# Performance work log

Measured on AMD Instinct MI355X. Metric: run time of the kernel, lower is better.

The kernel has to match this reference:

```python
import jax, jax.numpy as jnp
import numpy as np

D_MODEL = 1024
NUM_HEADS = 16
DEPTH = D_MODEL // NUM_HEADS
MAX_LEN = 5000


def _make_pe(d_model=D_MODEL, max_len=MAX_LEN):
    # Faithful to torch PositionalEncoding: pe shape [max_len, 1, d_model]
    position = np.arange(max_len, dtype=np.float32)[:, None]
    div_term = np.exp(np.arange(0, d_model, 2, dtype=np.float32) * (-np.log(10000.0) / d_model))
    pe = np.zeros((max_len, d_model), dtype=np.float32)
    pe[:, 0::2] = np.sin(position * div_term)
    pe[:, 1::2] = np.cos(position * div_term)
    return jnp.asarray(pe[:, None, :])  # [max_len, 1, d_model]


def setup_inputs() -> dict:
    key = jax.random.key(0)
    ks = jax.random.split(key, 11)
    B, S, D = 4, 2048, D_MODEL
    s = 1.0 / np.sqrt(D)
    inp = {
        "v": jax.random.normal(ks[0], (B, S, D), jnp.float32),
        "k": jax.random.normal(ks[1], (B, S, D), jnp.float32),
        "q": jax.random.normal(ks[2], (B, S, D), jnp.float32),
        "wq_w": jax.random.normal(ks[3], (D, D), jnp.float32) * s,
        "wq_b": jnp.zeros((D,), jnp.float32),
        "wk_w": jax.random.normal(ks[4], (D, D), jnp.float32) * s,
        "wk_b": jnp.zeros((D,), jnp.float32),
        "wv_w": jax.random.normal(ks[5], (D, D), jnp.float32) * s,
        "wv_b": jnp.zeros((D,), jnp.float32),
        "dense_w": jax.random.normal(ks[6], (D, D), jnp.float32) * s,
        "dense_b": jnp.zeros((D,), jnp.float32),
        "pe": _make_pe(),
    }
    return inp


def _split_heads(x, B):
    # [B, S, D] -> [B, H, S, depth]
    return x.reshape(B, -1, NUM_HEADS, DEPTH).transpose(0, 2, 1, 3)


def reference(v, k, q, wq_w, wq_b, wk_w, wk_b, wv_w, wv_b, dense_w, dense_b, pe):
    B = q.shape[0]
    # Faithful bug-reproduction: pe[:batch] has shape [B, 1, D], broadcast over seq.
    pe_b = pe[:B]  # [B, 1, D]
    q = q + pe_b
    k = k + pe_b
    v = v + pe_b
    # Linear layers (torch: x @ W.T + b)
    qh = _split_heads(q @ wq_w.T + wq_b, B)  # [B,H,Sq,d]
    kh = _split_heads(k @ wk_w.T + wk_b, B)  # [B,H,Sk,d]
    vh = _split_heads(v @ wv_w.T + wv_b, B)  # [B,H,Sk,d]
    scale = 1.0 / jnp.sqrt(jnp.float32(DEPTH))
    logits = jnp.einsum("bhqd,bhkd->bhqk", qh, kh) * scale
    attn = jax.nn.softmax(logits, axis=-1)
    out = jnp.einsum("bhqk,bhkd->bhqd", attn, vh)
    out = out.transpose(0, 2, 1, 3).reshape(B, -1, D_MODEL)
    return out @ dense_w.T + dense_b
```

## Files before the change

### kernel.cpp

```cpp
#include <hip/hip_runtime.h>
#include <hip/hip_bf16.h>

typedef short short8 __attribute__((ext_vector_type(8)));
typedef float f32x4 __attribute__((ext_vector_type(4)));
typedef float f32x16 __attribute__((ext_vector_type(16)));
typedef unsigned int uint4v __attribute__((ext_vector_type(4)));

#define MFMA16(a, b, c) __builtin_amdgcn_mfma_f32_16x16x32_bf16(a, b, c, 0, 0, 0)
#define MFMA32(a, b, c) __builtin_amdgcn_mfma_f32_32x32x16_bf16(a, b, c, 0, 0, 0)

typedef __attribute__((address_space(1))) const unsigned int gas_u32;
typedef __attribute__((address_space(3))) unsigned int las_u32;

__device__ inline void gll16(const void* g, void* l) {
    __builtin_amdgcn_global_load_lds((gas_u32*)g, (las_u32*)l, 16, 0, 0);
}

__device__ inline unsigned short f2bf(float f) {
    unsigned u = __builtin_bit_cast(unsigned, f);
    u += 0x7fff + ((u >> 16) & 1);
    return (unsigned short)(u >> 16);
}

__device__ inline unsigned pk_perm(float a, float b, unsigned sel) {
    unsigned r;
    asm("v_perm_b32 %0, %1, %2, %3"
        : "=v"(r)
        : "v"(__builtin_bit_cast(unsigned, b)), "v"(__builtin_bit_cast(unsigned, a)), "s"(sel));
    return r;
}

__device__ inline float exp2_fast(float x) {
#if __has_builtin(__builtin_amdgcn_exp2f)
    return __builtin_amdgcn_exp2f(x);
#else
    float r; asm("v_exp_f32 %0, %1" : "=v"(r) : "v"(x)); return r;
#endif
}

__device__ inline void pl32_swap(unsigned &a, unsigned &b) {
    asm volatile("v_permlane32_swap_b32 %0, %1" : "+v"(a), "+v"(b));
}

__global__ void pe_wcast(const float* __restrict__ q, const float* __restrict__ k,
                         const float* __restrict__ v, const float* __restrict__ pe,
                         const float* __restrict__ w0, const float* __restrict__ w1,
                         const float* __restrict__ w2, const float* __restrict__ w3,
                         unsigned short* __restrict__ oq, unsigned short* __restrict__ ok,
                         unsigned short* __restrict__ ov, unsigned short* __restrict__ ow) {
    if (blockIdx.y == 3) {
        if (blockIdx.x >= 4096) return;
        int wsel = blockIdx.x >> 10;
        const float* w = (wsel == 0) ? w0 : (wsel == 1) ? w1 : (wsel == 2) ? w2 : w3;
        unsigned short* o = ow + (size_t)wsel * 1024 * 1024;
        int i = (blockIdx.x & 1023) * 256 + threadIdx.x;
        float4 xv = reinterpret_cast<const float4*>(w)[i];
        ushort4 r;
        r.x = f2bf(xv.x); r.y = f2bf(xv.y); r.z = f2bf(xv.z); r.w = f2bf(xv.w);
        reinterpret_cast<ushort4*>(o)[i] = r;
        return;
    }
    const float* x = (blockIdx.y == 0) ? q : (blockIdx.y == 1) ? k : v;
    unsigned short* o = (blockIdx.y == 0) ? oq : (blockIdx.y == 1) ? ok : ov;
    int i = blockIdx.x * 256 + threadIdx.x;
    long e = (long)i * 4;
    int b = (int)(e >> 21);
    int d = (int)(e & 1023);
    float4 xv = reinterpret_cast<const float4*>(x)[i];
    float4 pv = *reinterpret_cast<const float4*>(pe + b * 1024 + d);
    ushort4 r;
    r.x = f2bf(xv.x + pv.x); r.y = f2bf(xv.y + pv.y);
    r.z = f2bf(xv.z + pv.z); r.w = f2bf(xv.w + pv.w);
    reinterpret_cast<ushort4*>(o)[i] = r;
}

__global__ __launch_bounds__(512, 2) void gemm8p(const unsigned short* __restrict__ A0,
                                                 const unsigned short* __restrict__ W0,
                                                 const float* __restrict__ bq,
                                                 const float* __restrict__ bk,
                                                 const float* __restrict__ bv,
                                                 unsigned short* __restrict__ oq,
                                                 unsigned short* __restrict__ ok,
                                                 unsigned short* __restrict__ ov,
                                                 float qscale) {
    const int NT = 16;
    __shared__ __align__(16) unsigned short lsA[2][256 * 64];
    __shared__ __align__(16) unsigned short lsB[2][256 * 64];

    int blk = blockIdx.x;
    int tid = threadIdx.x, wave = tid >> 6, lane = tid & 63;
    int lg = lane >> 4, l15 = lane & 15;
    int srow = tid >> 3;
    int scol = ((tid ^ srow) & 7) * 8;
    int swz_ = (l15 & 7) << 4;

    {
        int z = blk >> 7;
        int rem = blk & 127;
        int brow = (rem >> 2) * 256;
        int bcol = (rem & 3) * 256;
        const unsigned short* A = A0 + (size_t)z * 8192 * 1024;
        const unsigned short* W = W0 + (size_t)z * 1024 * 1024;
        const float* bias = (z == 0) ? bq : bk;
        float scale = (z == 0) ? qscale : 1.0f;
        unsigned short* out = (z == 0) ? oq : ok;

        int wr = wave >> 2, wc = wave & 3;
        const unsigned short* pA = A + (long)(brow + srow) * 1024 + scol;
        const unsigned short* pB = W + (long)(bcol + srow) * 1024 + scol;

        f32x4 acc[8][4];
#pragma unroll
        for (int m = 0; m < 8; ++m)
#pragma unroll
            for (int n = 0; n < 4; ++n) acc[m][n] = f32x4{0.f, 0.f, 0.f, 0.f};

#define SA(t, bi, q) gll16(pA + (t) * 64 + (q) * 65536,                     \
                           (char*)lsA[bi] + ((q) * 512 + wave * 64) * 16)
#define SB(t, bi, q) gll16(pB + (t) * 64 + (q) * 65536,                     \
                           (char*)lsB[bi] + ((q) * 512 + wave * 64) * 16)

        SB(0, 0, 0); SB(0, 0, 1); SB(0, 0, 2); SB(0, 0, 3);
        SA(0, 0, 0); SA(0, 0, 2); SA(0, 0, 1); SA(0, 0, 3);
        asm volatile("s_waitcnt vmcnt(2)" ::: "memory");
        __builtin_amdgcn_s_barrier();

        for (int t = 0; t < NT; ++t) {
            int cb = t & 1, nb = cb ^ 1;
            const char* KA = (const char*)lsA[cb];
            const char* KB = (const char*)lsB[cb];
            short8 af0[4][2], af1[4][2], bf0[2][2], bf1[2][2];
            const bool st = (t < NT - 1);

#pragma unroll
            for (int m = 0; m < 4; ++m)
#pragma unroll
                for (int kk = 0; kk < 2; ++kk)
                    af0[m][kk] = *(const short8*)(KA + (wr * 128 + m * 16 + l15) * 128 +
                                                  (((kk * 4 + lg) << 4) ^ swz_));
#pragma unroll
            for (int n = 0; n < 2; ++n)
#pragma unroll
                for (int kk = 0; kk < 2; ++kk)
                    bf0[n][kk] = *(const short8*)(KB + (wc * 64 + n * 16 + l15) * 128 +
                                                  (((kk * 4 + lg) << 4) ^ swz_));
            if (st) { SB(t + 1, nb, 0); SB(t + 1, nb, 1); }
            __builtin_amdgcn_s_barrier();
            asm volatile("s_waitcnt lgkmcnt(0)" ::: "memory");
            __builtin_amdgcn_s_setprio(1);
#pragma unroll
            for (int m = 0; m < 4; ++m)
#pragma unroll
                for (int n = 0; n < 2; ++n)
#pragma unroll
                    for (int kk = 0; kk < 2; ++kk)
                        acc[m][n] = MFMA16(af0[m][kk], bf0[n][kk], acc[m][n]);
            __builtin_amdgcn_s_setprio(0);
            __builtin_amdgcn_s_barrier();

#pragma unroll
            for (int n = 0; n < 2; ++n)
#pragma unroll
                for (int kk = 0; kk < 2; ++kk)
                    bf1[n][kk] = *(const short8*)(KB + (wc * 64 + (n + 2) * 16 + l15) * 128 +
                                                  (((kk * 4 + lg) << 4) ^ swz_));
            if (st) { SB(t + 1, nb, 2); SB(t + 1, nb, 3); }
            if (st) { asm volatile("s_waitcnt vmcnt(4)" ::: "memory"); }
            else    { asm volatile("s_waitcnt vmcnt(0)" ::: "memory"); }
            __builtin_amdgcn_s_barrier();
            asm volatile("s_waitcnt lgkmcnt(0)" ::: "memory");
            __builtin_amdgcn_s_setprio(1);
#pragma unroll
            for (int m = 0; m < 4; ++m)
#pragma unroll
                for (int n = 0; n < 2; ++n)
#pragma unroll
                    for (int kk = 0; kk < 2; ++kk)
                        acc[m][n + 2] = MFMA16(af0[m][kk], bf1[n][kk], acc[m][n + 2]);
            __builtin_amdgcn_s_setprio(0);
            __builtin_amdgcn_s_barrier();

#pragma unroll
            for (int m = 0; m < 4; ++m)
#pragma unroll
                for (int kk = 0; kk < 2; ++kk)
                    af1[m][kk] = *(const short8*)(KA + (wr * 128 + (m + 4) * 16 + l15) * 128 +
                                                  (((kk * 4 + lg) << 4) ^ swz_));
            if (st) { SA(t + 1, nb, 0); SA(t + 1, nb, 2); }
            __builtin_amdgcn_s_barrier();
            asm volatile("s_waitcnt lgkmcnt(0)" ::: "memory");
            __builtin_amdgcn_s_setprio(1);
#pragma unroll
            for (int m = 0; m < 4; ++m)
#pragma unroll
                for (int n = 0; n < 2; ++n)
#pragma unroll
                    for (int kk = 0; kk < 2; ++kk)
                        acc[m + 4][n] = MFMA16(af1[m][kk], bf0[n][kk], acc[m + 4][n]);
            __builtin_amdgcn_s_setprio(0);
            __builtin_amdgcn_s_barrier();

            if (st) {
                SA(t + 1, nb, 1); SA(t + 1, nb, 3);
                asm volatile("s_waitcnt vmcnt(2)" ::: "memory");
            }
            __builtin_amdgcn_s_barrier();
            __builtin_amdgcn_s_setprio(1);
#pragma unroll
            for (int m = 0; m < 4; ++m)
#pragma unroll
                for (int n = 0; n < 2; ++n)
#pragma unroll
                    for (int kk = 0; kk < 2; ++kk)
                        acc[m + 4][n + 2] = MFMA16(af1[m][kk], bf1[n][kk], acc[m + 4][n + 2]);
            __builtin_amdgcn_s_setprio(0);
            __builtin_amdgcn_s_barrier();
        }
#undef SA
#undef SB

#pragma unroll
        for (int m = 0; m < 8; ++m)
#pragma unroll
            for (int n = 0; n < 4; ++n) {
                int col = bcol + wc * 64 + n * 16 + l15;
                float bv_ = bias[col];
                int row0 = brow + wr * 128 + m * 16 + lg * 4;
#pragma unroll
                for (int r = 0; r < 4; ++r) {
                    int row = row0 + r;
                    float v = (acc[m][n][r] + bv_) * scale;
                    int b = row >> 11, s = row & 2047, h = col >> 6, d = col & 63;
                    out[(((long)(b * 16 + h) * 2048 + s) * 64 + d)] = f2bf(v);
                }
            }
    }

    {
        int ti = blk >> 1;
        int brow = (ti >> 2) * 256;
        int bcol = (ti & 3) * 256 + (blk & 1) * 128;
        const unsigned short* A = A0 + (size_t)2 * 8192 * 1024;
        const unsigned short* W = W0 + (size_t)2 * 1024 * 1024;

        int wr = wave >> 2, wc = wave & 3;
        const unsigned short* pA = A + (long)(brow + srow) * 1024 + scol;
        const unsigned short* pB = W + (long)(bcol + srow) * 1024 + scol;

        f32x4 acc[8][2];
#pragma unroll
        for (int m = 0; m < 8; ++m)
#pragma unroll
            for (int n = 0; n < 2; ++n) acc[m][n] = f32x4{0.f, 0.f, 0.f, 0.f};

#define SA2(t, bi, q) gll16(pA + (t) * 64 + (q) * 65536,                     \
                            (char*)lsA[bi] + ((q) * 512 + wave * 64) * 16)
#define SB2(t, bi, q) gll16(pB + (t) * 64 + (q) * 65536,                     \
                            (char*)lsB[bi] + ((q) * 512 + wave * 64) * 16)

        SB2(0, 0, 0); SB2(0, 0, 1); SA2(0, 0, 0); SA2(0, 0, 2);
        SA2(0, 0, 1); SA2(0, 0, 3);
        asm volatile("s_waitcnt vmcnt(2)" ::: "memory");
        __builtin_amdgcn_s_barrier();

        for (int t = 0; t < NT; ++t) {
            int cb = t & 1, nb = cb ^ 1;
            const char* KA = (const char*)lsA[cb];
            const char* KB = (const char*)lsB[cb];
            const bool st = (t < NT - 1);
            short8 af[8][2], bf[2][2];

#pragma unroll
            for (int m = 0; m < 4; ++m)
#pragma unroll
                for (int kk = 0; kk < 2; ++kk)
                    af[m][kk] = *(const short8*)(KA + (wr * 128 + m * 16 + l15) * 128 +
                                                 (((kk * 4 + lg) << 4) ^ swz_));
#pragma unroll
            for (int n = 0; n < 2; ++n)
#pragma unroll
                for (int kk = 0; kk < 2; ++kk)
                    bf[n][kk] = *(const short8*)(KB + (wc * 32 + n * 16 + l15) * 128 +
                                                 (((kk * 4 + lg) << 4) ^ swz_));
            if (st) { SB2(t + 1, nb, 0); SB2(t + 1, nb, 1); SA2(t + 1, nb, 0); SA2(t + 1, nb, 2); }
            __builtin_amdgcn_s_barrier();
            asm volatile("s_waitcnt lgkmcnt(0)" ::: "memory");
            __builtin_amdgcn_s_setprio(1);
#pragma unroll
            for (int m = 0; m < 4; ++m)
#pragma unroll
                for (int n = 0; n < 2; ++n)
#pragma unroll
                    for (int kk = 0; kk < 2; ++kk)
                        acc[m][n] = MFMA16(af[m][kk], bf[n][kk], acc[m][n]);
            __builtin_amdgcn_s_setprio(0);
            if (st) { asm volatile("s_waitcnt vmcnt(4)" ::: "memory"); }
            else    { asm volatile("s_waitcnt vmcnt(0)" ::: "memory"); }
            __builtin_amdgcn_s_barrier();

#pragma unroll
            for (int m = 4; m < 8; ++m)
#pragma unroll
                for (int kk = 0; kk < 2; ++kk)
                    af[m][kk] = *(const short8*)(KA + (wr * 128 + m * 16 + l15) * 128 +
                                                 (((kk * 4 + lg) << 4) ^ swz_));
            if (st) { SA2(t + 1, nb, 1); SA2(t + 1, nb, 3); }
            __builtin_amdgcn_s_barrier();
            asm volatile("s_waitcnt lgkmcnt(0)" ::: "memory");
            __builtin_amdgcn_s_setprio(1);
#pragma unroll
            for (int m = 4; m < 8; ++m)
#pragma unroll
                for (int n = 0; n < 2; ++n)
#pragma unroll
                    for (int kk = 0; kk < 2; ++kk)
                        acc[m][n] = MFMA16(af[m][kk], bf[n][kk], acc[m][n]);
            __builtin_amdgcn_s_setprio(0);
            if (st) { asm volatile("s_waitcnt vmcnt(2)" ::: "memory"); }
            __builtin_amdgcn_s_barrier();
        }
#undef SA2
#undef SB2

#pragma unroll
        for (int m = 0; m < 8; ++m)
#pragma unroll
            for (int n = 0; n < 2; ++n) {
                int col = bcol + wc * 32 + n * 16 + l15;
                float bv_ = bv[col];
                int row0 = brow + wr * 128 + m * 16 + lg * 4;
                int b = row0 >> 11, s0 = row0 & 2047;
                ushort4 pk;
                pk.x = f2bf(acc[m][n][0] + bv_);
                pk.y = f2bf(acc[m][n][1] + bv_);
                pk.z = f2bf(acc[m][n][2] + bv_);
                pk.w = f2bf(acc[m][n][3] + bv_);
                *(ushort4*)(ov + ((long)(b * 1024 + col)) * 2048 + s0) = pk;
            }
    }
}

__global__ __launch_bounds__(256, 3) void gemm_dense(const unsigned short* __restrict__ A,
                                                     const unsigned short* __restrict__ W,
                                                     const float* __restrict__ bias,
                                                     float* __restrict__ out) {
    const int NT = 32;
    __shared__ unsigned short lsA[3][128 * 32];
    __shared__ unsigned short lsB[3][128 * 32];

    int flat = blockIdx.x;
    int xcd = flat & 7;
    int s = flat >> 3;
    int brow = (xcd * 8 + (s & 7)) * 128;
    int bcol = (s >> 3) * 128;

    int tid = threadIdx.x;
    int wave = tid >> 6, lane = tid & 63, lg = lane >> 4, l15 = lane & 15;
    int wr = wave >> 1, wc = wave & 1;

    int c0 = wave * 64 + lane, c1 = 256 + c0;
    const unsigned short* sA0 = A + (long)(brow + (c0 >> 2)) * 1024 + ((c0 ^ (c0 >> 2)) & 3) * 8;
    const unsigned short* sA1 = A + (long)(brow + (c1 >> 2)) * 1024 + ((c1 ^ (c1 >> 2)) & 3) * 8;
    const unsigned short* sB0 = W + (long)(bcol + (c0 >> 2)) * 1024 + ((c0 ^ (c0 >> 2)) & 3) * 8;
    const unsigned short* sB1 = W + (long)(bcol + (c1 >> 2)) * 1024 + ((c1 ^ (c1 >> 2)) & 3) * 8;

    int cread = (lg * 16) ^ ((l15 & 3) << 4);

    f32x4 acc[4][4];
#pragma unroll
    for (int m = 0; m < 4; ++m)
#pragma unroll
        for (int n = 0; n < 4; ++n) acc[m][n] = f32x4{0.f, 0.f, 0.f, 0.f};

#define STG(k0, bi) do {                                                  \
        gll16(sA0 + (k0), (char*)lsA[bi] + (wave * 64) * 16);             \
        gll16(sA1 + (k0), (char*)lsA[bi] + (256 + wave * 64) * 16);       \
        gll16(sB0 + (k0), (char*)lsB[bi] + (wave * 64) * 16);             \
        gll16(sB1 + (k0), (char*)lsB[bi] + (256 + wave * 64) * 16);       \
    } while (0)

    STG(0, 0);
    STG(32, 1);

    int bi = 0, sb = 2;
    for (int t = 0; t < NT; ++t) {
        if (t == NT - 1) { asm volatile("s_waitcnt vmcnt(0)" ::: "memory"); }
        else             { asm volatile("s_waitcnt vmcnt(4)" ::: "memory"); }
        __builtin_amdgcn_s_barrier();
        if (t < NT - 2) STG((t + 2) * 32, sb);

        const char* KA = (const char*)lsA[bi];
        const char* KB = (const char*)lsB[bi];
        short8 af[4], bf_[4];
#pragma unroll
        for (int m = 0; m < 4; ++m) {
            int row = wr * 64 + m * 16 + l15;
            af[m] = *(const short8*)(KA + row * 64 + cread);
        }
#pragma unroll
        for (int n = 0; n < 4; ++n) {
            int col = wc * 64 + n * 16 + l15;
            bf_[n] = *(const short8*)(KB + col * 64 + cread);
        }
        __builtin_amdgcn_s_setprio(1);
#pragma unroll
        for (int m = 0; m < 4; ++m)
#pragma unroll
            for (int n = 0; n < 4; ++n) acc[m][n] = MFMA16(af[m], bf_[n], acc[m][n]);
        __builtin_amdgcn_s_setprio(0);

        bi = (bi == 2) ? 0 : bi + 1;
        sb = (sb == 2) ? 0 : sb + 1;
    }
#undef STG

#pragma unroll
    for (int m = 0; m < 4; ++m)
#pragma unroll
        for (int n = 0; n < 4; ++n) {
            int col = bcol + wc * 64 + n * 16 + l15;
            float bv_ = bias[col];
#pragma unroll
            for (int r = 0; r < 4; ++r) {
                int row = brow + wr * 64 + m * 16 + lg * 4 + r;
                out[(long)row * 1024 + col] = acc[m][n][r] + bv_;
            }
        }
}

__global__ __launch_bounds__(256, 2) void attn_kernel(const unsigned short* __restrict__ Qh,
                                                      const unsigned short* __restrict__ Kh,
                                                      const unsigned short* __restrict__ Vt,
                                                      unsigned short* __restrict__ Om) {
    const int S = 2048;
    const int NT = S / 64;
    int flat = blockIdx.x;
    int nf_ = (flat & 7) * 64 + (flat >> 3);
    int qt = nf_ & 7;
    int bh = nf_ >> 3;
    int b = bh >> 4, h = bh & 15;

    int tid = threadIdx.x, wave = tid >> 6, lane = tid & 63;
    int l31 = lane & 31, hi = lane >> 5;

    __shared__ __align__(16) unsigned short Kl[3][4096];
    __shared__ __align__(16) unsigned short Vtl[3][4096];

    const unsigned short* Qb = Qh + (long)bh * S * 64;
    const unsigned short* Kb = Kh + (long)bh * S * 64;
    const unsigned short* Vb = Vt + (long)bh * 64 * S;

    int colS = ((((tid & 7) * 16) ^ (((tid >> 3) & 7) << 4)) >> 1);
    const unsigned short* srcK = Kb + (tid >> 3) * 64 + colS;
    const unsigned short* srcV = Vb + (tid >> 3) * 2048 + colS;

    short8 aq[2][4];
    {
        const unsigned short* qrow = Qb + (long)(qt * 256 + wave * 64 + l31) * 64 + hi * 8;
#pragma unroll
        for (int qf = 0; qf < 2; ++qf)
#pragma unroll
            for (int s = 0; s < 4; ++s)
                aq[qf][s] = *(const short8*)(qrow + qf * 32 * 64 + s * 16);
    }

    f32x16 oacc[2][2], lacc[2], z16;
#pragma unroll
    for (int r = 0; r < 16; ++r) {
        oacc[0][0][r] = 0.f; oacc[0][1][r] = 0.f;
        oacc[1][0][r] = 0.f; oacc[1][1][r] = 0.f;
        lacc[0][r] = 0.f; lacc[1][r] = 0.f;
        z16[r] = 0.f;
    }

    const short8 ones8 = {0x3F80, 0x3F80, 0x3F80, 0x3F80, 0x3F80, 0x3F80, 0x3F80, 0x3F80};
    const unsigned SEL = 0x07060302u;

    int rb0 = l31 * 128;
    int swz = (l31 & 7) << 4;

#define STAGE(kt, bi) do {                                              \
        const unsigned short* sk = srcK + (kt) * 4096;                  \
        gll16(sk,         (char*)Kl[bi] + wave * 1024);                 \
        gll16(sk + 2048,  (char*)Kl[bi] + 4096 + wave * 1024);          \
        const unsigned short* sv = srcV + (kt) * 64;                    \
        gll16(sv,         (char*)Vtl[bi] + wave * 1024);                \
        gll16(sv + 65536, (char*)Vtl[bi] + 4096 + wave * 1024);         \
    } while (0)

    STAGE(0, 0);
    STAGE(1, 1);

    int bi = 0, sb = 2;
    for (int kt = 0; kt < NT; ++kt) {
        if (kt == NT - 1) { asm volatile("s_waitcnt vmcnt(0)" ::: "memory"); }
        else              { asm volatile("s_waitcnt vmcnt(4)" ::: "memory"); }
        __builtin_amdgcn_s_barrier();
        if (kt < NT - 2) STAGE(kt + 2, sb);

        const char* KlC = (const char*)Kl[bi];
        const char* VlC = (const char*)Vtl[bi];

        f32x16 sacc[2][2];
        __builtin_amdgcn_s_setprio(1);
#pragma unroll
        for (int blk = 0; blk < 2; ++blk) {
            short8 kf0 = *(const short8*)(KlC + blk * 4096 + rb0 + ((16 * hi) ^ swz));
            sacc[0][blk] = MFMA32(kf0, aq[0][0], z16);
            sacc[1][blk] = MFMA32(kf0, aq[1][0], z16);
#pragma unroll
            for (int s = 1; s < 4; ++s) {
                short8 kf = *(const short8*)(KlC + blk * 4096 + rb0 + ((32 * s + 16 * hi) ^ swz));
                sacc[0][blk] = MFMA32(kf, aq[0][s], sacc[0][blk]);
                sacc[1][blk] = MFMA32(kf, aq[1][s], sacc[1][blk]);
            }
        }
        __builtin_amdgcn_s_setprio(0);

#pragma unroll
        for (int qf = 0; qf < 2; ++qf)
#pragma unroll
            for (int blk = 0; blk < 2; ++blk)
#pragma unroll
                for (int r = 0; r < 16; ++r) sacc[qf][blk][r] = exp2_fast(sacc[qf][blk][r]);

#pragma unroll
        for (int s = 0; s < 4; ++s) {
            const int blk = s >> 1, base = (s & 1) * 8;
            short8 pa[2];
#pragma unroll
            for (int qf = 0; qf < 2; ++qf) {
                unsigned q0 = pk_perm(sacc[qf][blk][base + 0], sacc[qf][blk][base + 1], SEL);
                unsigned q1 = pk_perm(sacc[qf][blk][base + 2], sacc[qf][blk][base + 3], SEL);
                unsigned q2 = pk_perm(sacc[qf][blk][base + 4], sacc[qf][blk][base + 5], SEL);
                unsigned q3 = pk_perm(sacc[qf][blk][base + 6], sacc[qf][blk][base + 7], SEL);
                pl32_swap(q0, q2);
                pl32_swap(q1, q3);
                uint4v pw; pw[0] = q0; pw[1] = q1; pw[2] = q2; pw[3] = q3;
                pa[qf] = __builtin_bit_cast(short8, pw);
            }
            __builtin_amdgcn_s_setprio(1);
#pragma unroll
            for (int dblk = 0; dblk < 2; ++dblk) {
                short8 vf = *(const short8*)(VlC + dblk * 4096 + rb0 + ((32 * s + 16 * hi) ^ swz));
                oacc[0][dblk] = MFMA32(pa[0], vf, oacc[0][dblk]);
                oacc[1][dblk] = MFMA32(pa[1], vf, oacc[1][dblk]);
            }
            lacc[0] = MFMA32(pa[0], ones8, lacc[0]);
            lacc[1] = MFMA32(pa[1], ones8, lacc[1]);
            __builtin_amdgcn_s_setprio(0);
        }
        bi = (bi == 2) ? 0 : bi + 1;
        sb = (sb == 2) ? 0 : sb + 1;
    }
#undef STAGE

#pragma unroll
    for (int qf = 0; qf < 2; ++qf) {
        float inv[16];
#pragma unroll
        for (int r = 0; r < 16; ++r) inv[r] = 1.0f / lacc[qf][r];
        int qrow0 = qt * 256 + wave * 64 + qf * 32 + 4 * hi;
#pragma unroll
        for (int dblk = 0; dblk < 2; ++dblk)
#pragma unroll
            for (int r = 0; r < 16; ++r) {
                int qrow = qrow0 + (r & 3) + 8 * (r >> 2);
                int d = h * 64 + dblk * 32 + l31;
                float v = oacc[qf][dblk][r] * inv[r];
                Om[((long)b * 2048 + qrow) * 1024 + d] = f2bf(v);
            }
    }
}

extern "C" void kernel_launch(void* const* d_in, const int* in_sizes, int n_in,
                              void* d_out, int out_size, void* d_ws, size_t ws_size,
                              hipStream_t stream) {
    const float* v_in = (const float*)d_in[0];
    const float* k_in = (const float*)d_in[1];
    const float* q_in = (const float*)d_in[2];
    const float* wq_w = (const float*)d_in[3];
    const float* wq_b = (const float*)d_in[4];
    const float* wk_w = (const float*)d_in[5];
    const float* wk_b = (const float*)d_in[6];
    const float* wv_w = (const float*)d_in[7];
    const float* wv_b = (const float*)d_in[8];
    const float* wd_w = (const float*)d_in[9];
    const float* wd_b = (const float*)d_in[10];
    const float* pe   = (const float*)d_in[11];

    const long SZ = 8192L * 1024 * 2;
    char* ws = (char*)d_ws;
    unsigned short* xq = (unsigned short*)(ws + 0);
    unsigned short* xk = (unsigned short*)(ws + SZ);
    unsigned short* xv = (unsigned short*)(ws + 2 * SZ);
    unsigned short* qh = (unsigned short*)(ws + 3 * SZ);
    unsigned short* kh = (unsigned short*)(ws + 4 * SZ);
    unsigned short* vt = (unsigned short*)(ws + 5 * SZ);
    unsigned short* wqb16 = (unsigned short*)(ws + 6 * SZ);

    pe_wcast<<<dim3(8192, 4), 256, 0, stream>>>(q_in, k_in, v_in, pe,
                                                wq_w, wk_w, wv_w, wd_w,
                                                xq, xk, xv, wqb16);

    const float QSCALE = 0.125f * 1.44269504088896f;
    gemm8p<<<256, 512, 0, stream>>>(
        xq, wqb16, wq_b, wk_b, wv_b, qh, kh, vt, QSCALE);

    unsigned short* om = xq;
    attn_kernel<<<512, 256, 0, stream>>>(qh, kh, vt, om);

    gemm_dense<<<512, 256, 0, stream>>>(
        om, wqb16 + 3L * 1024 * 1024, wd_b, (float*)d_out);
}
```

Measured before the change: 201.1 us.

## Triple-buffer V projection GEMM to prefetch two K-tiles ahead

```diff
diff --git a/kernel.cpp b/kernel.cpp
--- a/kernel.cpp
+++ b/kernel.cpp
@@ -84,8 +84,7 @@
                                                  unsigned short* __restrict__ ov,
                                                  float qscale) {
     const int NT = 16;
-    __shared__ __align__(16) unsigned short lsA[2][256 * 64];
-    __shared__ __align__(16) unsigned short lsB[2][256 * 64];
+    __shared__ __align__(16) char smem[147456];
 
     int blk = blockIdx.x;
     int tid = threadIdx.x, wave = tid >> 6, lane = tid & 63;
@@ -115,10 +114,12 @@
 #pragma unroll
             for (int n = 0; n < 4; ++n) acc[m][n] = f32x4{0.f, 0.f, 0.f, 0.f};
 
+#define LSA1(b) (smem + (b) * 32768)
+#define LSB1(b) (smem + 65536 + (b) * 32768)
 #define SA(t, bi, q) gll16(pA + (t) * 64 + (q) * 65536,                     \
-                           (char*)lsA[bi] + ((q) * 512 + wave * 64) * 16)
+                           LSA1(bi) + ((q) * 512 + wave * 64) * 16)
 #define SB(t, bi, q) gll16(pB + (t) * 64 + (q) * 65536,                     \
-                           (char*)lsB[bi] + ((q) * 512 + wave * 64) * 16)
+                           LSB1(bi) + ((q) * 512 + wave * 64) * 16)
 
         SB(0, 0, 0); SB(0, 0, 1); SB(0, 0, 2); SB(0, 0, 3);
         SA(0, 0, 0); SA(0, 0, 2); SA(0, 0, 1); SA(0, 0, 3);
@@ -127,8 +128,8 @@
 
         for (int t = 0; t < NT; ++t) {
             int cb = t & 1, nb = cb ^ 1;
-            const char* KA = (const char*)lsA[cb];
-            const char* KB = (const char*)lsB[cb];
+            const char* KA = (const char*)LSA1(cb);
+            const char* KB = (const char*)LSB1(cb);
             short8 af0[4][2], af1[4][2], bf0[2][2], bf1[2][2];
             const bool st = (t < NT - 1);
 
@@ -218,6 +219,8 @@
         }
 #undef SA
 #undef SB
+#undef LSA1
+#undef LSB1
 
 #pragma unroll
         for (int m = 0; m < 8; ++m)
@@ -253,21 +256,25 @@
 #pragma unroll
             for (int n = 0; n < 2; ++n) acc[m][n] = f32x4{0.f, 0.f, 0.f, 0.f};
 
+#define LSA2(b) (smem + (b) * 32768)
+#define LSB2(b) (smem + 98304 + (b) * 16384)
 #define SA2(t, bi, q) gll16(pA + (t) * 64 + (q) * 65536,                     \
-                            (char*)lsA[bi] + ((q) * 512 + wave * 64) * 16)
+                            LSA2(bi) + ((q) * 512 + wave * 64) * 16)
 #define SB2(t, bi, q) gll16(pB + (t) * 64 + (q) * 65536,                     \
-                            (char*)lsB[bi] + ((q) * 512 + wave * 64) * 16)
-
-        SB2(0, 0, 0); SB2(0, 0, 1); SA2(0, 0, 0); SA2(0, 0, 2);
-        SA2(0, 0, 1); SA2(0, 0, 3);
-        asm volatile("s_waitcnt vmcnt(2)" ::: "memory");
+                            LSB2(bi) + ((q) * 512 + wave * 64) * 16)
+#define ISSUE6(t, bi) do { SB2(t, bi, 0); SB2(t, bi, 1); SA2(t, bi, 0);      \
+                           SA2(t, bi, 2); SA2(t, bi, 1); SA2(t, bi, 3); } while (0)
+
+        ISSUE6(0, 0);
+        ISSUE6(1, 1);
+        asm volatile("s_waitcnt vmcnt(6)" ::: "memory");
         __builtin_amdgcn_s_barrier();
 
         for (int t = 0; t < NT; ++t) {
-            int cb = t & 1, nb = cb ^ 1;
-            const char* KA = (const char*)lsA[cb];
-            const char* KB = (const char*)lsB[cb];
-            const bool st = (t < NT - 1);
+            int cb = t % 3, pf = (t + 2) % 3;
+            const char* KA = (const char*)LSA2(cb);
+            const char* KB = (const char*)LSB2(cb);
+            const bool st = (t < NT - 2);
             short8 af[8][2], bf[2][2];
 
 #pragma unroll
@@ -282,7 +289,7 @@
                 for (int kk = 0; kk < 2; ++kk)
                     bf[n][kk] = *(const short8*)(KB + (wc * 32 + n * 16 + l15) * 128 +
                                                  (((kk * 4 + lg) << 4) ^ swz_));
-            if (st) { SB2(t + 1, nb, 0); SB2(t + 1, nb, 1); SA2(t + 1, nb, 0); SA2(t + 1, nb, 2); }
+            if (st) { SB2(t + 2, pf, 0); SB2(t + 2, pf, 1); SA2(t + 2, pf, 0); SA2(t + 2, pf, 2); }
             __builtin_amdgcn_s_barrier();
             asm volatile("s_waitcnt lgkmcnt(0)" ::: "memory");
             __builtin_amdgcn_s_setprio(1);
@@ -294,8 +301,6 @@
                     for (int kk = 0; kk < 2; ++kk)
                         acc[m][n] = MFMA16(af[m][kk], bf[n][kk], acc[m][n]);
             __builtin_amdgcn_s_setprio(0);
-            if (st) { asm volatile("s_waitcnt vmcnt(4)" ::: "memory"); }
-            else    { asm volatile("s_waitcnt vmcnt(0)" ::: "memory"); }
             __builtin_amdgcn_s_barrier();
 
 #pragma unroll
@@ -304,7 +309,7 @@
                 for (int kk = 0; kk < 2; ++kk)
                     af[m][kk] = *(const short8*)(KA + (wr * 128 + m * 16 + l15) * 128 +
                                                  (((kk * 4 + lg) << 4) ^ swz_));
-            if (st) { SA2(t + 1, nb, 1); SA2(t + 1, nb, 3); }
+            if (st) { SA2(t + 2, pf, 1); SA2(t + 2, pf, 3); }
             __builtin_amdgcn_s_barrier();
             asm volatile("s_waitcnt lgkmcnt(0)" ::: "memory");
             __builtin_amdgcn_s_setprio(1);
@@ -316,11 +321,15 @@
                     for (int kk = 0; kk < 2; ++kk)
                         acc[m][n] = MFMA16(af[m][kk], bf[n][kk], acc[m][n]);
             __builtin_amdgcn_s_setprio(0);
-            if (st) { asm volatile("s_waitcnt vmcnt(2)" ::: "memory"); }
+            if (t < NT - 2)      { asm volatile("s_waitcnt vmcnt(6)" ::: "memory"); }
+            else if (t == NT - 2){ asm volatile("s_waitcnt vmcnt(0)" ::: "memory"); }
             __builtin_amdgcn_s_barrier();
         }
+#undef ISSUE6
 #undef SA2
 #undef SB2
+#undef LSA2
+#undef LSB2
 
 #pragma unroll
         for (int m = 0; m < 8; ++m)
```

Result: no change. 203.5 us (+1.2%).
